# Kernel tuning notes

Hardware: AMD Instinct MI355X
Metric: run time of the kernel (lower is better)

## Reference

```python
import jax, jax.numpy as jnp
import numpy as np

B, P, M, C = 64, 8732, 16, 81
THRESHOLD = 0.5
NEG_POS_RATIO = 3
ALPHA = 1.0  # config.reg_weights
EPS = 1e-7


def cxcy_to_xy(c):
    return jnp.concatenate([c[..., :2] - c[..., 2:] / 2.0,
                            c[..., :2] + c[..., 2:] / 2.0], axis=-1)


def _rand_boxes_cxcy(key, shape):
    k1, k2 = jax.random.split(key)
    cxcy = jax.random.uniform(k1, shape + (2,), minval=0.2, maxval=0.8)
    wh = jax.random.uniform(k2, shape + (2,), minval=0.05, maxval=0.35)
    return jnp.concatenate([cxcy, wh], axis=-1)


def setup_inputs() -> dict:
    key = jax.random.key(0)
    ks = jax.random.split(key, 5)
    predicted_locs = cxcy_to_xy(_rand_boxes_cxcy(ks[0], (B, P)))          # valid corner boxes
    predicted_scores = jax.random.normal(ks[1], (B, P, C), dtype=jnp.float32)
    boxes = jnp.clip(cxcy_to_xy(_rand_boxes_cxcy(ks[2], (B, M))), 0.0, 1.0)  # GT corner boxes
    labels = jax.random.randint(ks[3], (B, M), 1, C)                       # object labels (1..C-1)
    priors_cxcy = _rand_boxes_cxcy(ks[4], (P,))
    return {"predicted_locs": predicted_locs, "predicted_scores": predicted_scores,
            "boxes": boxes, "labels": labels, "priors_cxcy": priors_cxcy}


def jaccard(a, b):
    # a: [M,4], b: [P,4] corner boxes -> [M,P] IoU
    lt = jnp.maximum(a[:, None, :2], b[None, :, :2])
    rb = jnp.minimum(a[:, None, 2:], b[None, :, 2:])
    wh = jnp.clip(rb - lt, 0.0)
    inter = wh[..., 0] * wh[..., 1]
    area_a = (a[:, 2] - a[:, 0]) * (a[:, 3] - a[:, 1])
    area_b = (b[:, 2] - b[:, 0]) * (b[:, 3] - b[:, 1])
    return inter / (area_a[:, None] + area_b[None, :] - inter)


def diou_loss(b1, b2):
    # corner boxes, elementwise over leading dims -> per-box loss 1 - DIoU
    lt = jnp.maximum(b1[..., :2], b2[..., :2])
    rb = jnp.minimum(b1[..., 2:], b2[..., 2:])
    wh = jnp.clip(rb - lt, 0.0)
    inter = wh[..., 0] * wh[..., 1]
    area1 = (b1[..., 2] - b1[..., 0]) * (b1[..., 3] - b1[..., 1])
    area2 = (b2[..., 2] - b2[..., 0]) * (b2[..., 3] - b2[..., 1])
    iou = inter / (area1 + area2 - inter + EPS)
    c1 = (b1[..., :2] + b1[..., 2:]) / 2.0
    c2 = (b2[..., :2] + b2[..., 2:]) / 2.0
    inter_diag = jnp.sum((c1 - c2) ** 2, axis=-1)
    enc_lt = jnp.minimum(b1[..., :2], b2[..., :2])
    enc_rb = jnp.maximum(b1[..., 2:], b2[..., 2:])
    outer_diag = jnp.sum((enc_rb - enc_lt) ** 2, axis=-1)
    dious = jnp.clip(iou - inter_diag / (outer_diag + EPS), -1.0, 1.0)
    return 1.0 - dious


def reference(predicted_locs, predicted_scores, boxes, labels, priors_cxcy):
    priors_xy = cxcy_to_xy(priors_cxcy)

    def assign(boxes_i, labels_i):
        overlap = jaccard(boxes_i, priors_xy)              # [M, P]
        ovl_prior = overlap.max(axis=0)                    # best overlap per prior
        obj_prior = overlap.argmax(axis=0)                 # best object per prior
        ovl_obj = overlap.max(axis=1)                      # best overlap per object
        prior_obj = overlap.argmax(axis=1)                 # best prior per object
        valid = ovl_obj > 0
        j_idx = jnp.cumsum(valid.astype(jnp.int32)) - 1    # index within filtered list (faithful)
        idx = jnp.where(valid, prior_obj, P)               # P -> dropped (out of bounds)
        ovl_prior = ovl_prior.at[idx].set(1.0, mode='drop')
        obj_prior = obj_prior.at[idx].set(j_idx, mode='drop')
        lab = labels_i[obj_prior]
        label_pos = jnp.where(ovl_prior < THRESHOLD, 0, lab)
        label_neg = jnp.where(ovl_prior < THRESHOLD - 0.1, -1, lab)
        return label_pos, label_neg

    true_classes, true_neg_classes = jax.vmap(assign)(boxes, labels)  # [B,P] each
    positive = true_classes > 0                                        # [B,P]
    pos_f = positive.astype(jnp.float32)
    n_pos_total = jnp.sum(pos_f)

    # Localization loss: DIoU(pred_pos, pred_pos) with reduce='mean' (faithful to source)
    per_box = diou_loss(predicted_locs, predicted_locs)                # [B,P]
    loc_loss = jnp.sum(per_box * pos_f) / jnp.maximum(n_pos_total, 1.0)

    # Confidence loss: per-prior CE + hard-negative mining (neg_pos_ratio)
    logp = jax.nn.log_softmax(predicted_scores, axis=-1)
    conf_all = -jnp.take_along_axis(logp, true_classes[..., None], axis=-1)[..., 0]  # [B,P]
    conf_pos_sum = jnp.sum(conf_all * pos_f)
    conf_neg = jnp.where(positive, 0.0, conf_all)
    conf_neg_sorted = -jnp.sort(-conf_neg, axis=-1)                    # descending
    n_hard = NEG_POS_RATIO * jnp.sum(positive, axis=1)                 # [B]
    hard_mask = (jnp.arange(P)[None, :] < n_hard[:, None]).astype(jnp.float32)
    conf_loss = (jnp.sum(conf_neg_sorted * hard_mask) + conf_pos_sum) / n_pos_total

    return conf_loss + ALPHA * loc_loss
```

## Files before the change

kernel.cpp:

```cpp
#include <hip/hip_runtime.h>
#include <math.h>

#define B_ 64
#define P_ 8732
#define M_ 16
#define C_ 81
#define THRESH 0.5f
#define EPS_ 1e-7f

#define ROWS_PER_CHUNK 64
#define NCHUNKS ((B_ * P_) / ROWS_PER_CHUNK)
#define CHUNK_F4 (ROWS_PER_CHUNK * C_ / 4)

__global__ __launch_bounds__(1024) void assign_kernel(
    const float* __restrict__ boxes,
    const int*   __restrict__ labels,
    const float* __restrict__ priors,
    int*         __restrict__ true_classes,
    int*         __restrict__ n_pos,
    int*         __restrict__ done_ctr)
{
    const int b = blockIdx.x;
    const int tid = threadIdx.x;
    const int lane = tid & 63;
    const int wv = tid >> 6;

    if (b == 0 && tid == 0) *done_ctr = 0;

    __shared__ float s_ovl[P_];
    __shared__ unsigned char s_obj[P_];
    __shared__ float s_bx[M_][4];
    __shared__ float s_barea[M_];
    __shared__ int   s_lab[M_];
    __shared__ float s_wv[M_][16];
    __shared__ int   s_wp[M_][16];
    __shared__ float s_ovl_obj[M_];
    __shared__ int   s_prior_obj[M_];
    __shared__ int   s_cnt[16];

    if (tid < M_*4) ((float*)s_bx)[tid] = boxes[b*M_*4 + tid];
    if (tid < M_)   s_lab[tid] = labels[b*M_ + tid];
    __syncthreads();
    if (tid < M_)
        s_barea[tid] = (s_bx[tid][2]-s_bx[tid][0])*(s_bx[tid][3]-s_bx[tid][1]);
    __syncthreads();

    float bestv[M_]; int bestp[M_];
    #pragma unroll
    for (int m = 0; m < M_; ++m) { bestv[m] = -1.0f; bestp[m] = 0x7fffffff; }

    for (int p = tid; p < P_; p += 1024) {
        float4 pc = ((const float4*)priors)[p];
        float px1 = pc.x - pc.z*0.5f, py1 = pc.y - pc.w*0.5f;
        float px2 = pc.x + pc.z*0.5f, py2 = pc.y + pc.w*0.5f;
        float parea = (px2-px1)*(py2-py1);
        float bv = -1.0f; int bm = 0;
        #pragma unroll
        for (int m = 0; m < M_; ++m) {
            float ix1 = fmaxf(s_bx[m][0], px1);
            float iy1 = fmaxf(s_bx[m][1], py1);
            float ix2 = fminf(s_bx[m][2], px2);
            float iy2 = fminf(s_bx[m][3], py2);
            float iw = fmaxf(ix2-ix1, 0.0f);
            float ih = fmaxf(iy2-iy1, 0.0f);
            float inter = iw*ih;
            float iou = inter / (s_barea[m] + parea - inter);
            if (iou > bv) { bv = iou; bm = m; }
            if (iou > bestv[m]) { bestv[m] = iou; bestp[m] = p; }
        }
        s_ovl[p] = bv;
        s_obj[p] = (unsigned char)bm;
    }

    #pragma unroll
    for (int m = 0; m < M_; ++m) {
        float v = bestv[m]; int p = bestp[m];
        #pragma unroll
        for (int o = 32; o; o >>= 1) {
            float v2 = __shfl_xor(v, o);
            int   p2 = __shfl_xor(p, o);
            if (v2 > v || (v2 == v && p2 < p)) { v = v2; p = p2; }
        }
        if (lane == 0) { s_wv[m][wv] = v; s_wp[m][wv] = p; }
    }
    __syncthreads();

    if (tid < M_) {
        float v = s_wv[tid][0]; int p = s_wp[tid][0];
        #pragma unroll
        for (int w = 1; w < 16; ++w) {
            float v2 = s_wv[tid][w]; int p2 = s_wp[tid][w];
            if (v2 > v || (v2 == v && p2 < p)) { v = v2; p = p2; }
        }
        s_ovl_obj[tid] = v; s_prior_obj[tid] = p;
    }
    __syncthreads();

    if (tid == 0) {
        int cnt = 0;
        for (int m = 0; m < M_; ++m) {
            if (s_ovl_obj[m] > 0.0f) {
                int p = s_prior_obj[m];
                s_ovl[p] = 1.0f;
                s_obj[p] = (unsigned char)cnt;
                cnt++;
            }
        }
    }
    __syncthreads();

    int cpos = 0;
    for (int p = tid; p < P_; p += 1024) {
        int tc = 0;
        if (!(s_ovl[p] < THRESH)) tc = s_lab[s_obj[p]];
        true_classes[(size_t)b*P_ + p] = tc;
        cpos += (tc > 0);
    }
    #pragma unroll
    for (int o = 32; o; o >>= 1) cpos += __shfl_xor(cpos, o);
    if (lane == 0) s_cnt[wv] = cpos;
    __syncthreads();
    if (tid == 0) {
        int t = 0;
        #pragma unroll
        for (int w = 0; w < 16; ++w) t += s_cnt[w];
        n_pos[b] = t;
    }
}

__global__ __launch_bounds__(256, 6) void ce_loc_kernel(
    const float* __restrict__ scores,
    const float* __restrict__ locs,
    const int*   __restrict__ tcls,
    float*       __restrict__ conf_neg,
    float*       __restrict__ blk_pos,
    float*       __restrict__ blk_loc)
{
    const int c    = blockIdx.x;
    const int tid  = threadIdx.x;
    const int lane = tid & 63;
    const int wv   = tid >> 6;
    const int s    = lane & 3;
    const int rl   = (lane >> 2) + wv * 16;

    __shared__ __attribute__((aligned(16))) float s_buf[ROWS_PER_CHUNK * C_];
    __shared__ float s_red[4][2];

    const float4* src4 = (const float4*)scores + (size_t)c * CHUNK_F4;
    float4*       dst4 = (float4*)s_buf;

    #pragma unroll
    for (int k = 0; k < 5; ++k) {
        __builtin_amdgcn_global_load_lds(
            (const __attribute__((address_space(1))) void*)(src4 + k*256 + tid),
            (__attribute__((address_space(3))) void*)(dst4 + k*256 + wv*64),
            16, 0, 0);
    }
    if (tid < 16) dst4[1280 + tid] = src4[1280 + tid];

    const int row = c * ROWS_PER_CHUNK + rl;
    const int t = tcls[row];
    __syncthreads();

    const int cnt   = (s == 0) ? 21 : 20;
    const int cbase = (s == 0) ? 0  : (1 + 20 * s);

    const float* rowp = &s_buf[rl * C_ + cbase];
    float x[21];
    float mx = -INFINITY;
    #pragma unroll
    for (int k = 0; k < 21; ++k) {
        if (k < cnt) { x[k] = rowp[k]; mx = fmaxf(mx, x[k]); }
        else x[k] = -INFINITY;
    }
    mx = fmaxf(mx, __shfl_xor(mx, 1));
    mx = fmaxf(mx, __shfl_xor(mx, 2));

    float e = 0.f, stv = 0.f;
    #pragma unroll
    for (int k = 0; k < 21; ++k) {
        e += __expf(x[k] - mx);
        if ((cbase + k == t) && (k < cnt)) stv = x[k];
    }
    e   += __shfl_xor(e, 1);   e   += __shfl_xor(e, 2);
    stv += __shfl_xor(stv, 1); stv += __shfl_xor(stv, 2);

    float p_acc = 0.f, l_acc = 0.f;
    if (s == 0) {
        float conf = mx + __logf(e) - stv;
        if (t > 0) {
            conf_neg[row] = 0.f;
            p_acc = conf;
            float4 bx = ((const float4*)locs)[row];
            float w = bx.z - bx.x, h = bx.w - bx.y;
            float iw = fmaxf(w, 0.f), ih = fmaxf(h, 0.f);
            float inter = iw * ih;
            float area  = w * h;
            float iou   = inter / (area + area - inter + EPS_);
            float diou  = fminf(fmaxf(iou, -1.f), 1.f);
            l_acc = 1.f - diou;
        } else {
            conf_neg[row] = fmaxf(conf, 0.f);
        }
    }

    #pragma unroll
    for (int o = 32; o; o >>= 1) {
        p_acc += __shfl_xor(p_acc, o);
        l_acc += __shfl_xor(l_acc, o);
    }
    if (lane == 0) { s_red[wv][0] = p_acc; s_red[wv][1] = l_acc; }
    __syncthreads();
    if (tid == 0) {
        blk_pos[c] = s_red[0][0] + s_red[1][0] + s_red[2][0] + s_red[3][0];
        blk_loc[c] = s_red[0][1] + s_red[1][1] + s_red[2][1] + s_red[3][1];
    }
}

__global__ __launch_bounds__(1024) void topk_kernel(
    const float* __restrict__ conf_neg,
    const int*   __restrict__ n_pos,
    const float* __restrict__ blk_pos,
    const float* __restrict__ blk_loc,
    float*       __restrict__ hard,
    int*         __restrict__ done_ctr,
    float*       __restrict__ out)
{
    const int b = blockIdx.x;
    const int tid = threadIdx.x;
    const int lane = tid & 63;
    const int wv = tid >> 6;

    __shared__ float s_v[P_];
    __shared__ int   s_hist[16][256];
    __shared__ int   s_cg[257];
    __shared__ int   s_sel;
    __shared__ int   s_t[16];
    __shared__ float s_f[16];
    __shared__ int   s_last;
    __shared__ double sd[16][4];

    const float4* cn4 = (const float4*)(conf_neg + (size_t)b * P_);
    for (int i = tid; i < P_/4; i += 1024) ((float4*)s_v)[i] = cn4[i];

    int k = 3 * n_pos[b];
    if (k > P_) k = P_;

    float hsum = 0.f;
    if (k > 0) {
        __syncthreads();

        const unsigned masks[4]  = {0u, 0xFF800000u, 0xFFFF8000u, 0xFFFFFF80u};
        const int      shifts[4] = {23, 15, 7, 0};

        unsigned prefix = 0u;
        int k_rem = k;

        for (int rd = 0; rd < 4; ++rd) {
            const unsigned hm = masks[rd];
            const int sh = shifts[rd];

            ((int*)s_hist)[tid] = 0;
            ((int*)s_hist)[tid + 1024] = 0;
            ((int*)s_hist)[tid + 2048] = 0;
            ((int*)s_hist)[tid + 3072] = 0;
            __syncthreads();

            for (int i = tid; i < P_; i += 1024) {
                unsigned u = __float_as_uint(s_v[i]);
                if ((u & hm) == prefix)
                    atomicAdd(&s_hist[wv][(u >> sh) & 0xFF], 1);
            }
            __syncthreads();

            if (wv == 0) {
                int carry = 0;
                for (int cbin = 3; cbin >= 0; --cbin) {
                    int bin = cbin * 64 + lane;
                    int tot = 0;
                    #pragma unroll
                    for (int w = 0; w < 16; ++w) tot += s_hist[w][bin];
                    #pragma unroll
                    for (int o = 1; o < 64; o <<= 1) {
                        int v = __shfl_down(tot, o);
                        if (lane + o < 64) tot += v;
                    }
                    int cg = tot + carry;
                    s_cg[bin] = cg;
                    carry = __shfl(cg, 0);
                }
                if (lane == 0) s_cg[256] = 0;
            }
            __syncthreads();

            if (tid < 256) {
                if (s_cg[tid] >= k_rem && s_cg[tid + 1] < k_rem) s_sel = tid;
            }
            __syncthreads();

            const int bsel = s_sel;
            k_rem -= s_cg[bsel + 1];
            prefix |= (unsigned)bsel << sh;
            __syncthreads();
        }

        const float tval = __uint_as_float(prefix);

        float sum = 0.f; int cgt = 0;
        for (int i = tid; i < P_; i += 1024) {
            float v = s_v[i];
            if (v > tval) { sum += v; cgt++; }
        }
        #pragma unroll
        for (int o = 32; o; o >>= 1) { sum += __shfl_xor(sum, o); cgt += __shfl_xor(cgt, o); }
        if (lane == 0) { s_f[wv] = sum; s_t[wv] = cgt; }
        __syncthreads();
        if (tid == 0) {
            float ssum = 0.f; int cc = 0;
            #pragma unroll
            for (int w = 0; w < 16; ++w) { ssum += s_f[w]; cc += s_t[w]; }
            hsum = ssum + (float)(k - cc) * tval;
        }
    }

    if (tid == 0) {
        atomicExch(&hard[b], hsum);
        __threadfence();
        s_last = (atomicAdd(done_ctr, 1) == B_ - 1) ? 1 : 0;
    }
    __syncthreads();

    if (s_last) {
        __threadfence();
        double p = 0.0, l = 0.0;
        for (int i = tid; i < NCHUNKS; i += 1024) { p += blk_pos[i]; l += blk_loc[i]; }
        double h = 0.0, np = 0.0;
        if (tid < B_) {
            h  = (double)atomicAdd(&hard[tid], 0.0f);
            np = (double)n_pos[tid];
        }
        #pragma unroll
        for (int o = 32; o; o >>= 1) {
            p += __shfl_xor(p, o); l += __shfl_xor(l, o);
            h += __shfl_xor(h, o); np += __shfl_xor(np, o);
        }
        if (lane == 0) { sd[wv][0] = p; sd[wv][1] = l; sd[wv][2] = h; sd[wv][3] = np; }
        __syncthreads();
        if (tid == 0) {
            double tp = 0, tl = 0, th = 0, tn = 0;
            #pragma unroll
            for (int w = 0; w < 16; ++w) { tp += sd[w][0]; tl += sd[w][1]; th += sd[w][2]; tn += sd[w][3]; }
            double conf_loss = (th + tp) / tn;
            double loc_loss  = tl / fmax(tn, 1.0);
            out[0] = (float)(conf_loss + 1.0 * loc_loss);
        }
    }
}

extern "C" void kernel_launch(void* const* d_in, const int* in_sizes, int n_in,
                              void* d_out, int out_size, void* d_ws, size_t ws_size,
                              hipStream_t stream) {
    const float* predicted_locs   = (const float*)d_in[0];
    const float* predicted_scores = (const float*)d_in[1];
    const float* boxes            = (const float*)d_in[2];
    const int*   labels           = (const int*)d_in[3];
    const float* priors           = (const float*)d_in[4];
    float* out = (float*)d_out;

    char* ws = (char*)d_ws;
    size_t off = 0;
    int*    true_classes = (int*)(ws + off);   off += sizeof(int)   * (size_t)B_ * P_;
    float*  conf_neg     = (float*)(ws + off); off += sizeof(float) * (size_t)B_ * P_;
    float*  blk_pos      = (float*)(ws + off); off += sizeof(float) * NCHUNKS;
    float*  blk_loc      = (float*)(ws + off); off += sizeof(float) * NCHUNKS;
    float*  hard         = (float*)(ws + off); off += sizeof(float) * B_;
    int*    n_pos        = (int*)(ws + off);   off += sizeof(int)   * B_;
    int*    done_ctr     = (int*)(ws + off);   off += sizeof(int)   * 4;

    assign_kernel<<<B_, 1024, 0, stream>>>(boxes, labels, priors,
                                           true_classes, n_pos, done_ctr);
    ce_loc_kernel<<<NCHUNKS, 256, 0, stream>>>(predicted_scores, predicted_locs,
                                               true_classes, conf_neg,
                                               blk_pos, blk_loc);
    topk_kernel<<<B_, 1024, 0, stream>>>(conf_neg, n_pos, blk_pos, blk_loc,
                                         hard, done_ctr, out);
}
```

Measured before the change: 361.2 us.

## Fuse assignment with log-sum-exp kernel and move CE gather into top-k

The prior-to-box assignment now runs in the same grid as the per-row log-sum-exp pass. The first 64 blocks do the assignment and the remaining blocks compute only the LSE, so the LSE no longer waits on true_classes and one kernel launch plus the serial dependency go away. The assignment blocks shrink to 256 threads and compute IoU twice instead of holding per-prior overlap in shared memory. The top-k kernel now gathers the target score, computes the positive CE and localization sums and counts positives itself, so the per-chunk partial buffers and the conf_neg array are dropped. The cost is scattered gathers from the scores tensor inside the top-k kernel and fewer threads per block on the assignment path.

```diff
diff --git a/kernel.cpp b/kernel.cpp
--- a/kernel.cpp
+++ b/kernel.cpp
@@ -8,221 +8,176 @@
 #define THRESH 0.5f
 #define EPS_ 1e-7f
 
+#define AB_ 64
 #define ROWS_PER_CHUNK 64
 #define NCHUNKS ((B_ * P_) / ROWS_PER_CHUNK)
 #define CHUNK_F4 (ROWS_PER_CHUNK * C_ / 4)
 
-__global__ __launch_bounds__(1024) void assign_kernel(
+__global__ __launch_bounds__(256, 4) void fused_assign_lse(
+    const float* __restrict__ scores,
     const float* __restrict__ boxes,
     const int*   __restrict__ labels,
     const float* __restrict__ priors,
-    int*         __restrict__ true_classes,
-    int*         __restrict__ n_pos,
+    float*       __restrict__ lse,
+    int*         __restrict__ tcls,
     int*         __restrict__ done_ctr)
 {
-    const int b = blockIdx.x;
-    const int tid = threadIdx.x;
-    const int lane = tid & 63;
-    const int wv = tid >> 6;
-
-    if (b == 0 && tid == 0) *done_ctr = 0;
-
-    __shared__ float s_ovl[P_];
-    __shared__ unsigned char s_obj[P_];
+    __shared__ __attribute__((aligned(16))) float s_buf[ROWS_PER_CHUNK * C_];
     __shared__ float s_bx[M_][4];
     __shared__ float s_barea[M_];
     __shared__ int   s_lab[M_];
-    __shared__ float s_wv[M_][16];
-    __shared__ int   s_wp[M_][16];
-    __shared__ float s_ovl_obj[M_];
-    __shared__ int   s_prior_obj[M_];
-    __shared__ int   s_cnt[16];
-
-    if (tid < M_*4) ((float*)s_bx)[tid] = boxes[b*M_*4 + tid];
-    if (tid < M_)   s_lab[tid] = labels[b*M_ + tid];
-    __syncthreads();
-    if (tid < M_)
-        s_barea[tid] = (s_bx[tid][2]-s_bx[tid][0])*(s_bx[tid][3]-s_bx[tid][1]);
-    __syncthreads();
-
-    float bestv[M_]; int bestp[M_];
-    #pragma unroll
-    for (int m = 0; m < M_; ++m) { bestv[m] = -1.0f; bestp[m] = 0x7fffffff; }
-
-    for (int p = tid; p < P_; p += 1024) {
-        float4 pc = ((const float4*)priors)[p];
-        float px1 = pc.x - pc.z*0.5f, py1 = pc.y - pc.w*0.5f;
-        float px2 = pc.x + pc.z*0.5f, py2 = pc.y + pc.w*0.5f;
-        float parea = (px2-px1)*(py2-py1);
-        float bv = -1.0f; int bm = 0;
-        #pragma unroll
-        for (int m = 0; m < M_; ++m) {
-            float ix1 = fmaxf(s_bx[m][0], px1);
-            float iy1 = fmaxf(s_bx[m][1], py1);
-            float ix2 = fminf(s_bx[m][2], px2);
-            float iy2 = fminf(s_bx[m][3], py2);
-            float iw = fmaxf(ix2-ix1, 0.0f);
-            float ih = fmaxf(iy2-iy1, 0.0f);
-            float inter = iw*ih;
-            float iou = inter / (s_barea[m] + parea - inter);
-            if (iou > bv) { bv = iou; bm = m; }
-            if (iou > bestv[m]) { bestv[m] = iou; bestp[m] = p; }
-        }
-        s_ovl[p] = bv;
-        s_obj[p] = (unsigned char)bm;
-    }
-
-    #pragma unroll
-    for (int m = 0; m < M_; ++m) {
-        float v = bestv[m]; int p = bestp[m];
-        #pragma unroll
-        for (int o = 32; o; o >>= 1) {
-            float v2 = __shfl_xor(v, o);
-            int   p2 = __shfl_xor(p, o);
-            if (v2 > v || (v2 == v && p2 < p)) { v = v2; p = p2; }
-        }
-        if (lane == 0) { s_wv[m][wv] = v; s_wp[m][wv] = p; }
-    }
-    __syncthreads();
-
-    if (tid < M_) {
-        float v = s_wv[tid][0]; int p = s_wp[tid][0];
-        #pragma unroll
-        for (int w = 1; w < 16; ++w) {
-            float v2 = s_wv[tid][w]; int p2 = s_wp[tid][w];
-            if (v2 > v || (v2 == v && p2 < p)) { v = v2; p = p2; }
-        }
-        s_ovl_obj[tid] = v; s_prior_obj[tid] = p;
-    }
-    __syncthreads();
-
-    if (tid == 0) {
-        int cnt = 0;
-        for (int m = 0; m < M_; ++m) {
-            if (s_ovl_obj[m] > 0.0f) {
-                int p = s_prior_obj[m];
-                s_ovl[p] = 1.0f;
-                s_obj[p] = (unsigned char)cnt;
-                cnt++;
-            }
-        }
-    }
-    __syncthreads();
-
-    int cpos = 0;
-    for (int p = tid; p < P_; p += 1024) {
-        int tc = 0;
-        if (!(s_ovl[p] < THRESH)) tc = s_lab[s_obj[p]];
-        true_classes[(size_t)b*P_ + p] = tc;
-        cpos += (tc > 0);
-    }
-    #pragma unroll
-    for (int o = 32; o; o >>= 1) cpos += __shfl_xor(cpos, o);
-    if (lane == 0) s_cnt[wv] = cpos;
-    __syncthreads();
-    if (tid == 0) {
-        int t = 0;
-        #pragma unroll
-        for (int w = 0; w < 16; ++w) t += s_cnt[w];
-        n_pos[b] = t;
-    }
-}
-
-__global__ __launch_bounds__(256, 6) void ce_loc_kernel(
-    const float* __restrict__ scores,
-    const float* __restrict__ locs,
-    const int*   __restrict__ tcls,
-    float*       __restrict__ conf_neg,
-    float*       __restrict__ blk_pos,
-    float*       __restrict__ blk_loc)
-{
-    const int c    = blockIdx.x;
+    __shared__ float s_wv4[M_][4];
+    __shared__ int   s_wp4[M_][4];
+    __shared__ int   s_tp[M_];
+    __shared__ int   s_tn;
+
     const int tid  = threadIdx.x;
     const int lane = tid & 63;
     const int wv   = tid >> 6;
-    const int s    = lane & 3;
-    const int rl   = (lane >> 2) + wv * 16;
-
-    __shared__ __attribute__((aligned(16))) float s_buf[ROWS_PER_CHUNK * C_];
-    __shared__ float s_red[4][2];
-
-    const float4* src4 = (const float4*)scores + (size_t)c * CHUNK_F4;
-    float4*       dst4 = (float4*)s_buf;
-
-    #pragma unroll
-    for (int k = 0; k < 5; ++k) {
-        __builtin_amdgcn_global_load_lds(
-            (const __attribute__((address_space(1))) void*)(src4 + k*256 + tid),
-            (__attribute__((address_space(3))) void*)(dst4 + k*256 + wv*64),
-            16, 0, 0);
-    }
-    if (tid < 16) dst4[1280 + tid] = src4[1280 + tid];
-
-    const int row = c * ROWS_PER_CHUNK + rl;
-    const int t = tcls[row];
-    __syncthreads();
-
-    const int cnt   = (s == 0) ? 21 : 20;
-    const int cbase = (s == 0) ? 0  : (1 + 20 * s);
-
-    const float* rowp = &s_buf[rl * C_ + cbase];
-    float x[21];
-    float mx = -INFINITY;
-    #pragma unroll
-    for (int k = 0; k < 21; ++k) {
-        if (k < cnt) { x[k] = rowp[k]; mx = fmaxf(mx, x[k]); }
-        else x[k] = -INFINITY;
-    }
-    mx = fmaxf(mx, __shfl_xor(mx, 1));
-    mx = fmaxf(mx, __shfl_xor(mx, 2));
-
-    float e = 0.f, stv = 0.f;
-    #pragma unroll
-    for (int k = 0; k < 21; ++k) {
-        e += __expf(x[k] - mx);
-        if ((cbase + k == t) && (k < cnt)) stv = x[k];
-    }
-    e   += __shfl_xor(e, 1);   e   += __shfl_xor(e, 2);
-    stv += __shfl_xor(stv, 1); stv += __shfl_xor(stv, 2);
-
-    float p_acc = 0.f, l_acc = 0.f;
-    if (s == 0) {
-        float conf = mx + __logf(e) - stv;
-        if (t > 0) {
-            conf_neg[row] = 0.f;
-            p_acc = conf;
-            float4 bx = ((const float4*)locs)[row];
-            float w = bx.z - bx.x, h = bx.w - bx.y;
-            float iw = fmaxf(w, 0.f), ih = fmaxf(h, 0.f);
-            float inter = iw * ih;
-            float area  = w * h;
-            float iou   = inter / (area + area - inter + EPS_);
-            float diou  = fminf(fmaxf(iou, -1.f), 1.f);
-            l_acc = 1.f - diou;
-        } else {
-            conf_neg[row] = fmaxf(conf, 0.f);
-        }
-    }
-
-    #pragma unroll
-    for (int o = 32; o; o >>= 1) {
-        p_acc += __shfl_xor(p_acc, o);
-        l_acc += __shfl_xor(l_acc, o);
-    }
-    if (lane == 0) { s_red[wv][0] = p_acc; s_red[wv][1] = l_acc; }
-    __syncthreads();
-    if (tid == 0) {
-        blk_pos[c] = s_red[0][0] + s_red[1][0] + s_red[2][0] + s_red[3][0];
-        blk_loc[c] = s_red[0][1] + s_red[1][1] + s_red[2][1] + s_red[3][1];
+
+    if (blockIdx.x < AB_) {
+        const int b = blockIdx.x;
+        if (b == 0 && tid == 0) *done_ctr = 0;
+
+        if (tid < M_*4) ((float*)s_bx)[tid] = boxes[b*M_*4 + tid];
+        if (tid < M_)   s_lab[tid] = labels[b*M_ + tid];
+        __syncthreads();
+        if (tid < M_)
+            s_barea[tid] = (s_bx[tid][2]-s_bx[tid][0])*(s_bx[tid][3]-s_bx[tid][1]);
+        __syncthreads();
+
+        const float4* pri4 = (const float4*)priors;
+
+        float bestv[M_]; int bestp[M_];
+        #pragma unroll
+        for (int m = 0; m < M_; ++m) { bestv[m] = -1.0f; bestp[m] = 0x7fffffff; }
+
+        for (int p = tid; p < P_; p += 256) {
+            float4 pc = pri4[p];
+            float px1 = pc.x - pc.z*0.5f, py1 = pc.y - pc.w*0.5f;
+            float px2 = pc.x + pc.z*0.5f, py2 = pc.y + pc.w*0.5f;
+            float parea = (px2-px1)*(py2-py1);
+            #pragma unroll
+            for (int m = 0; m < M_; ++m) {
+                float ix1 = fmaxf(s_bx[m][0], px1);
+                float iy1 = fmaxf(s_bx[m][1], py1);
+                float ix2 = fminf(s_bx[m][2], px2);
+                float iy2 = fminf(s_bx[m][3], py2);
+                float iw = fmaxf(ix2-ix1, 0.0f);
+                float ih = fmaxf(iy2-iy1, 0.0f);
+                float inter = iw*ih;
+                float iou = inter / (s_barea[m] + parea - inter);
+                if (iou > bestv[m]) { bestv[m] = iou; bestp[m] = p; }
+            }
+        }
+
+        #pragma unroll
+        for (int m = 0; m < M_; ++m) {
+            float v = bestv[m]; int p = bestp[m];
+            #pragma unroll
+            for (int o = 32; o; o >>= 1) {
+                float v2 = __shfl_xor(v, o);
+                int   p2 = __shfl_xor(p, o);
+                if (v2 > v || (v2 == v && p2 < p)) { v = v2; p = p2; }
+            }
+            if (lane == 0) { s_wv4[m][wv] = v; s_wp4[m][wv] = p; }
+        }
+        __syncthreads();
+
+        if (tid == 0) {
+            int cnt = 0;
+            for (int m = 0; m < M_; ++m) {
+                float v = s_wv4[m][0]; int p = s_wp4[m][0];
+                #pragma unroll
+                for (int w = 1; w < 4; ++w) {
+                    float v2 = s_wv4[m][w]; int p2 = s_wp4[m][w];
+                    if (v2 > v || (v2 == v && p2 < p)) { v = v2; p = p2; }
+                }
+                if (v > 0.0f) { s_tp[cnt] = p; cnt++; }
+            }
+            s_tn = cnt;
+        }
+        __syncthreads();
+
+        const int tn = s_tn;
+
+        for (int p = tid; p < P_; p += 256) {
+            float4 pc = pri4[p];
+            float px1 = pc.x - pc.z*0.5f, py1 = pc.y - pc.w*0.5f;
+            float px2 = pc.x + pc.z*0.5f, py2 = pc.y + pc.w*0.5f;
+            float parea = (px2-px1)*(py2-py1);
+            float bv = -1.0f; int bm = 0;
+            #pragma unroll
+            for (int m = 0; m < M_; ++m) {
+                float ix1 = fmaxf(s_bx[m][0], px1);
+                float iy1 = fmaxf(s_bx[m][1], py1);
+                float ix2 = fminf(s_bx[m][2], px2);
+                float iy2 = fminf(s_bx[m][3], py2);
+                float iw = fmaxf(ix2-ix1, 0.0f);
+                float ih = fmaxf(iy2-iy1, 0.0f);
+                float inter = iw*ih;
+                float iou = inter / (s_barea[m] + parea - inter);
+                if (iou > bv) { bv = iou; bm = m; }
+            }
+            int ovr = -1;
+            for (int e = 0; e < tn; ++e)
+                if (s_tp[e] == p) ovr = e;
+            int tc = (ovr >= 0) ? s_lab[ovr]
+                                : ((bv < THRESH) ? 0 : s_lab[bm]);
+            tcls[(size_t)b*P_ + p] = tc;
+        }
+    } else {
+        const int c  = blockIdx.x - AB_;
+        const int s  = lane & 3;
+        const int rl = (lane >> 2) + wv * 16;
+
+        const float4* src4 = (const float4*)scores + (size_t)c * CHUNK_F4;
+        float4*       dst4 = (float4*)s_buf;
+
+        #pragma unroll
+        for (int k = 0; k < 5; ++k) {
+            __builtin_amdgcn_global_load_lds(
+                (const __attribute__((address_space(1))) void*)(src4 + k*256 + tid),
+                (__attribute__((address_space(3))) void*)(dst4 + k*256 + wv*64),
+                16, 0, 0);
+        }
+        if (tid < 16) dst4[1280 + tid] = src4[1280 + tid];
+        __syncthreads();
+
+        const int cnt   = (s == 0) ? 21 : 20;
+        const int cbase = (s == 0) ? 0  : (1 + 20 * s);
+
+        const float* rowp = &s_buf[rl * C_ + cbase];
+        float x[21];
+        float mx = -INFINITY;
+        #pragma unroll
+        for (int k = 0; k < 21; ++k) {
+            if (k < cnt) { x[k] = rowp[k]; mx = fmaxf(mx, x[k]); }
+            else x[k] = -INFINITY;
+        }
+        mx = fmaxf(mx, __shfl_xor(mx, 1));
+        mx = fmaxf(mx, __shfl_xor(mx, 2));
+
+        float e = 0.f;
+        #pragma unroll
+        for (int k = 0; k < 21; ++k) e += __expf(x[k] - mx);
+        e += __shfl_xor(e, 1);
+        e += __shfl_xor(e, 2);
+
+        if (s == 0)
+            lse[(size_t)c * ROWS_PER_CHUNK + rl] = mx + __logf(e);
     }
 }
 
 __global__ __launch_bounds__(1024) void topk_kernel(
-    const float* __restrict__ conf_neg,
-    const int*   __restrict__ n_pos,
-    const float* __restrict__ blk_pos,
-    const float* __restrict__ blk_loc,
+    const float* __restrict__ scores,
+    const float* __restrict__ locs,
+    const float* __restrict__ lse,
+    const int*   __restrict__ tcls,
     float*       __restrict__ hard,
+    float*       __restrict__ psum,
+    float*       __restrict__ lsum,
+    int*         __restrict__ npos,
     int*         __restrict__ done_ctr,
     float*       __restrict__ out)
 {
@@ -235,21 +190,55 @@
     __shared__ int   s_hist[16][256];
     __shared__ int   s_cg[257];
     __shared__ int   s_sel;
-    __shared__ int   s_t[16];
-    __shared__ float s_f[16];
+    __shared__ int   s_ct[16];
+    __shared__ float s_pa[16];
+    __shared__ float s_la[16];
+    __shared__ int   s_rt[16];
+    __shared__ float s_rf[16];
     __shared__ int   s_last;
-    __shared__ double sd[16][4];
-
-    const float4* cn4 = (const float4*)(conf_neg + (size_t)b * P_);
-    for (int i = tid; i < P_/4; i += 1024) ((float4*)s_v)[i] = cn4[i];
-
-    int k = 3 * n_pos[b];
+
+    const size_t base = (size_t)b * P_;
+
+    float p_acc = 0.f, l_acc = 0.f; int cpos = 0;
+    for (int i = tid; i < P_; i += 1024) {
+        const int t = tcls[base + i];
+        const float conf = lse[base + i] - scores[(base + i) * C_ + t];
+        float v;
+        if (t > 0) {
+            v = 0.f;
+            cpos++;
+            p_acc += conf;
+            float4 bx = ((const float4*)locs)[base + i];
+            float w = bx.z - bx.x, h = bx.w - bx.y;
+            float iw = fmaxf(w, 0.f), ih = fmaxf(h, 0.f);
+            float inter = iw * ih;
+            float area  = w * h;
+            float iou   = inter / (area + area - inter + EPS_);
+            float diou  = fminf(fmaxf(iou, -1.f), 1.f);
+            l_acc += 1.f - diou;
+        } else {
+            v = fmaxf(conf, 0.f);
+        }
+        s_v[i] = v;
+    }
+
+    #pragma unroll
+    for (int o = 32; o; o >>= 1) {
+        cpos  += __shfl_xor(cpos, o);
+        p_acc += __shfl_xor(p_acc, o);
+        l_acc += __shfl_xor(l_acc, o);
+    }
+    if (lane == 0) { s_ct[wv] = cpos; s_pa[wv] = p_acc; s_la[wv] = l_acc; }
+    __syncthreads();
+
+    int cp_tot = 0;
+    #pragma unroll
+    for (int w = 0; w < 16; ++w) cp_tot += s_ct[w];
+    int k = 3 * cp_tot;
     if (k > P_) k = P_;
 
     float hsum = 0.f;
     if (k > 0) {
-        __syncthreads();
-
         const unsigned masks[4]  = {0u, 0xFF800000u, 0xFFFF8000u, 0xFFFFFF80u};
         const int      shifts[4] = {23, 15, 7, 0};
 
@@ -313,45 +302,43 @@
         }
         #pragma unroll
         for (int o = 32; o; o >>= 1) { sum += __shfl_xor(sum, o); cgt += __shfl_xor(cgt, o); }
-        if (lane == 0) { s_f[wv] = sum; s_t[wv] = cgt; }
+        if (lane == 0) { s_rf[wv] = sum; s_rt[wv] = cgt; }
         __syncthreads();
         if (tid == 0) {
             float ssum = 0.f; int cc = 0;
             #pragma unroll
-            for (int w = 0; w < 16; ++w) { ssum += s_f[w]; cc += s_t[w]; }
+            for (int w = 0; w < 16; ++w) { ssum += s_rf[w]; cc += s_rt[w]; }
             hsum = ssum + (float)(k - cc) * tval;
         }
     }
 
     if (tid == 0) {
+        float pt = 0.f, lt = 0.f;
+        #pragma unroll
+        for (int w = 0; w < 16; ++w) { pt += s_pa[w]; lt += s_la[w]; }
         atomicExch(&hard[b], hsum);
+        atomicExch(&psum[b], pt);
+        atomicExch(&lsum[b], lt);
+        atomicExch(&npos[b], cp_tot);
         __threadfence();
         s_last = (atomicAdd(done_ctr, 1) == B_ - 1) ? 1 : 0;
     }
     __syncthreads();
 
-    if (s_last) {
+    if (s_last && wv == 0) {
         __threadfence();
-        double p = 0.0, l = 0.0;
-        for (int i = tid; i < NCHUNKS; i += 1024) { p += blk_pos[i]; l += blk_loc[i]; }
-        double h = 0.0, np = 0.0;
-        if (tid < B_) {
-            h  = (double)atomicAdd(&hard[tid], 0.0f);
-            np = (double)n_pos[tid];
-        }
+        double h  = (double)atomicAdd(&hard[lane], 0.0f);
+        double p  = (double)atomicAdd(&psum[lane], 0.0f);
+        double l  = (double)atomicAdd(&lsum[lane], 0.0f);
+        double np = (double)atomicAdd(&npos[lane], 0);
         #pragma unroll
         for (int o = 32; o; o >>= 1) {
-            p += __shfl_xor(p, o); l += __shfl_xor(l, o);
-            h += __shfl_xor(h, o); np += __shfl_xor(np, o);
-        }
-        if (lane == 0) { sd[wv][0] = p; sd[wv][1] = l; sd[wv][2] = h; sd[wv][3] = np; }
-        __syncthreads();
-        if (tid == 0) {
-            double tp = 0, tl = 0, th = 0, tn = 0;
-            #pragma unroll
-            for (int w = 0; w < 16; ++w) { tp += sd[w][0]; tl += sd[w][1]; th += sd[w][2]; tn += sd[w][3]; }
-            double conf_loss = (th + tp) / tn;
-            double loc_loss  = tl / fmax(tn, 1.0);
+            h += __shfl_xor(h, o); p += __shfl_xor(p, o);
+            l += __shfl_xor(l, o); np += __shfl_xor(np, o);
+        }
+        if (lane == 0) {
+            double conf_loss = (h + p) / np;
+            double loc_loss  = l / fmax(np, 1.0);
             out[0] = (float)(conf_loss + 1.0 * loc_loss);
         }
     }
@@ -369,19 +356,17 @@
 
     char* ws = (char*)d_ws;
     size_t off = 0;
-    int*    true_classes = (int*)(ws + off);   off += sizeof(int)   * (size_t)B_ * P_;
-    float*  conf_neg     = (float*)(ws + off); off += sizeof(float) * (size_t)B_ * P_;
-    float*  blk_pos      = (float*)(ws + off); off += sizeof(float) * NCHUNKS;
-    float*  blk_loc      = (float*)(ws + off); off += sizeof(float) * NCHUNKS;
-    float*  hard         = (float*)(ws + off); off += sizeof(float) * B_;
-    int*    n_pos        = (int*)(ws + off);   off += sizeof(int)   * B_;
-    int*    done_ctr     = (int*)(ws + off);   off += sizeof(int)   * 4;
-
-    assign_kernel<<<B_, 1024, 0, stream>>>(boxes, labels, priors,
-                                           true_classes, n_pos, done_ctr);
-    ce_loc_kernel<<<NCHUNKS, 256, 0, stream>>>(predicted_scores, predicted_locs,
-                                               true_classes, conf_neg,
-                                               blk_pos, blk_loc);
-    topk_kernel<<<B_, 1024, 0, stream>>>(conf_neg, n_pos, blk_pos, blk_loc,
-                                         hard, done_ctr, out);
+    float* lse      = (float*)(ws + off); off += sizeof(float) * (size_t)B_ * P_;
+    int*   tcls     = (int*)(ws + off);   off += sizeof(int)   * (size_t)B_ * P_;
+    float* hard     = (float*)(ws + off); off += sizeof(float) * B_;
+    float* psum     = (float*)(ws + off); off += sizeof(float) * B_;
+    float* lsum     = (float*)(ws + off); off += sizeof(float) * B_;
+    int*   npos     = (int*)(ws + off);   off += sizeof(int)   * B_;
+    int*   done_ctr = (int*)(ws + off);   off += sizeof(int)   * 4;
+
+    fused_assign_lse<<<AB_ + NCHUNKS, 256, 0, stream>>>(
+        predicted_scores, boxes, labels, priors, lse, tcls, done_ctr);
+    topk_kernel<<<B_, 1024, 0, stream>>>(
+        predicted_scores, predicted_locs, lse, tcls,
+        hard, psum, lsum, npos, done_ctr, out);
 }
```

Measured after the change: 395.7 us. +9.6%, slower.

## Recompute IoU instead of LDS staging; grid-stride CE with 16 lanes per row

Applied to the files above, without the earlier changes.

The assign kernel drops its per-prior shared-memory overlap and object arrays and runs at 256 threads. It recomputes IoUs in a second pass and resolves forced matches with a small list lookup. The CE kernel replaces the LDS staging via global_load_lds with a persistent grid-stride loop over 2048 blocks. Each row is read straight from global memory by 16 lanes with shuffle reductions. This trades shared-memory footprint and launch count for extra recompute and less coalesced 81-float row loads. The top-k kernel's syncthreads moves outside the k>0 branch.

```diff
diff --git a/kernel.cpp b/kernel.cpp
--- a/kernel.cpp
+++ b/kernel.cpp
@@ -8,35 +8,31 @@
 #define THRESH 0.5f
 #define EPS_ 1e-7f
 
-#define ROWS_PER_CHUNK 64
-#define NCHUNKS ((B_ * P_) / ROWS_PER_CHUNK)
-#define CHUNK_F4 (ROWS_PER_CHUNK * C_ / 4)
-
-__global__ __launch_bounds__(1024) void assign_kernel(
+#define CE_BLOCKS 2048
+
+__global__ __launch_bounds__(256) void assign_kernel(
     const float* __restrict__ boxes,
     const int*   __restrict__ labels,
     const float* __restrict__ priors,
-    int*         __restrict__ true_classes,
+    int*         __restrict__ tcls,
     int*         __restrict__ n_pos,
-    int*         __restrict__ done_ctr)
+    int*         __restrict__ ctrs)
 {
-    const int b = blockIdx.x;
-    const int tid = threadIdx.x;
-    const int lane = tid & 63;
-    const int wv = tid >> 6;
-
-    if (b == 0 && tid == 0) *done_ctr = 0;
-
-    __shared__ float s_ovl[P_];
-    __shared__ unsigned char s_obj[P_];
     __shared__ float s_bx[M_][4];
     __shared__ float s_barea[M_];
     __shared__ int   s_lab[M_];
-    __shared__ float s_wv[M_][16];
-    __shared__ int   s_wp[M_][16];
-    __shared__ float s_ovl_obj[M_];
-    __shared__ int   s_prior_obj[M_];
-    __shared__ int   s_cnt[16];
+    __shared__ float s_wv4[M_][4];
+    __shared__ int   s_wp4[M_][4];
+    __shared__ int   s_tp[M_];
+    __shared__ int   s_tn;
+    __shared__ int   s_cnt[4];
+
+    const int b    = blockIdx.x;
+    const int tid  = threadIdx.x;
+    const int lane = tid & 63;
+    const int wv   = tid >> 6;
+
+    if (b == 0 && tid < 2) ctrs[tid] = 0;
 
     if (tid < M_*4) ((float*)s_bx)[tid] = boxes[b*M_*4 + tid];
     if (tid < M_)   s_lab[tid] = labels[b*M_ + tid];
@@ -44,13 +40,65 @@
     if (tid < M_)
         s_barea[tid] = (s_bx[tid][2]-s_bx[tid][0])*(s_bx[tid][3]-s_bx[tid][1]);
     __syncthreads();
+
+    const float4* pri4 = (const float4*)priors;
 
     float bestv[M_]; int bestp[M_];
     #pragma unroll
     for (int m = 0; m < M_; ++m) { bestv[m] = -1.0f; bestp[m] = 0x7fffffff; }
 
-    for (int p = tid; p < P_; p += 1024) {
-        float4 pc = ((const float4*)priors)[p];
+    for (int p = tid; p < P_; p += 256) {
+        float4 pc = pri4[p];
+        float px1 = pc.x - pc.z*0.5f, py1 = pc.y - pc.w*0.5f;
+        float px2 = pc.x + pc.z*0.5f, py2 = pc.y + pc.w*0.5f;
+        float parea = (px2-px1)*(py2-py1);
+        #pragma unroll
+        for (int m = 0; m < M_; ++m) {
+            float ix1 = fmaxf(s_bx[m][0], px1);
+            float iy1 = fmaxf(s_bx[m][1], py1);
+            float ix2 = fminf(s_bx[m][2], px2);
+            float iy2 = fminf(s_bx[m][3], py2);
+            float iw = fmaxf(ix2-ix1, 0.0f);
+            float ih = fmaxf(iy2-iy1, 0.0f);
+            float inter = iw*ih;
+            float iou = inter / (s_barea[m] + parea - inter);
+            if (iou > bestv[m]) { bestv[m] = iou; bestp[m] = p; }
+        }
+    }
+
+    #pragma unroll
+    for (int m = 0; m < M_; ++m) {
+        float v = bestv[m]; int p = bestp[m];
+        #pragma unroll
+        for (int o = 32; o; o >>= 1) {
+            float v2 = __shfl_xor(v, o);
+            int   p2 = __shfl_xor(p, o);
+            if (v2 > v || (v2 == v && p2 < p)) { v = v2; p = p2; }
+        }
+        if (lane == 0) { s_wv4[m][wv] = v; s_wp4[m][wv] = p; }
+    }
+    __syncthreads();
+
+    if (tid == 0) {
+        int cnt = 0;
+        for (int m = 0; m < M_; ++m) {
+            float v = s_wv4[m][0]; int p = s_wp4[m][0];
+            #pragma unroll
+            for (int w = 1; w < 4; ++w) {
+                float v2 = s_wv4[m][w]; int p2 = s_wp4[m][w];
+                if (v2 > v || (v2 == v && p2 < p)) { v = v2; p = p2; }
+            }
+            if (v > 0.0f) { s_tp[cnt] = p; cnt++; }
+        }
+        s_tn = cnt;
+    }
+    __syncthreads();
+
+    const int tn = s_tn;
+
+    int cpos = 0;
+    for (int p = tid; p < P_; p += 256) {
+        float4 pc = pri4[p];
         float px1 = pc.x - pc.z*0.5f, py1 = pc.y - pc.w*0.5f;
         float px2 = pc.x + pc.z*0.5f, py2 = pc.y + pc.w*0.5f;
         float parea = (px2-px1)*(py2-py1);
@@ -66,56 +114,16 @@
             float inter = iw*ih;
             float iou = inter / (s_barea[m] + parea - inter);
             if (iou > bv) { bv = iou; bm = m; }
-            if (iou > bestv[m]) { bestv[m] = iou; bestp[m] = p; }
-        }
-        s_ovl[p] = bv;
-        s_obj[p] = (unsigned char)bm;
-    }
-
-    #pragma unroll
-    for (int m = 0; m < M_; ++m) {
-        float v = bestv[m]; int p = bestp[m];
-        #pragma unroll
-        for (int o = 32; o; o >>= 1) {
-            float v2 = __shfl_xor(v, o);
-            int   p2 = __shfl_xor(p, o);
-            if (v2 > v || (v2 == v && p2 < p)) { v = v2; p = p2; }
-        }
-        if (lane == 0) { s_wv[m][wv] = v; s_wp[m][wv] = p; }
-    }
-    __syncthreads();
-
-    if (tid < M_) {
-        float v = s_wv[tid][0]; int p = s_wp[tid][0];
-        #pragma unroll
-        for (int w = 1; w < 16; ++w) {
-            float v2 = s_wv[tid][w]; int p2 = s_wp[tid][w];
-            if (v2 > v || (v2 == v && p2 < p)) { v = v2; p = p2; }
-        }
-        s_ovl_obj[tid] = v; s_prior_obj[tid] = p;
-    }
-    __syncthreads();
-
-    if (tid == 0) {
-        int cnt = 0;
-        for (int m = 0; m < M_; ++m) {
-            if (s_ovl_obj[m] > 0.0f) {
-                int p = s_prior_obj[m];
-                s_ovl[p] = 1.0f;
-                s_obj[p] = (unsigned char)cnt;
-                cnt++;
-            }
-        }
-    }
-    __syncthreads();
-
-    int cpos = 0;
-    for (int p = tid; p < P_; p += 1024) {
-        int tc = 0;
-        if (!(s_ovl[p] < THRESH)) tc = s_lab[s_obj[p]];
-        true_classes[(size_t)b*P_ + p] = tc;
+        }
+        int ovr = -1;
+        for (int e = 0; e < tn; ++e)
+            if (s_tp[e] == p) ovr = e;
+        int tc = (ovr >= 0) ? s_lab[ovr]
+                            : ((bv < THRESH) ? 0 : s_lab[bm]);
+        tcls[(size_t)b*P_ + p] = tc;
         cpos += (tc > 0);
     }
+
     #pragma unroll
     for (int o = 32; o; o >>= 1) cpos += __shfl_xor(cpos, o);
     if (lane == 0) s_cnt[wv] = cpos;
@@ -123,12 +131,12 @@
     if (tid == 0) {
         int t = 0;
         #pragma unroll
-        for (int w = 0; w < 16; ++w) t += s_cnt[w];
+        for (int w = 0; w < 4; ++w) t += s_cnt[w];
         n_pos[b] = t;
     }
 }
 
-__global__ __launch_bounds__(256, 6) void ce_loc_kernel(
+__global__ __launch_bounds__(256) void ce_loc_kernel(
     const float* __restrict__ scores,
     const float* __restrict__ locs,
     const int*   __restrict__ tcls,
@@ -136,71 +144,63 @@
     float*       __restrict__ blk_pos,
     float*       __restrict__ blk_loc)
 {
-    const int c    = blockIdx.x;
     const int tid  = threadIdx.x;
     const int lane = tid & 63;
+    const int j    = lane & 15;
+    const int g    = lane >> 4;
     const int wv   = tid >> 6;
-    const int s    = lane & 3;
-    const int rl   = (lane >> 2) + wv * 16;
-
-    __shared__ __attribute__((aligned(16))) float s_buf[ROWS_PER_CHUNK * C_];
+    const int gwave = blockIdx.x * 4 + wv;
+    const int ngrp  = CE_BLOCKS * 4;
+    const int NG = (B_ * P_) / 4;
+
     __shared__ float s_red[4][2];
 
-    const float4* src4 = (const float4*)scores + (size_t)c * CHUNK_F4;
-    float4*       dst4 = (float4*)s_buf;
-
-    #pragma unroll
-    for (int k = 0; k < 5; ++k) {
-        __builtin_amdgcn_global_load_lds(
-            (const __attribute__((address_space(1))) void*)(src4 + k*256 + tid),
-            (__attribute__((address_space(3))) void*)(dst4 + k*256 + wv*64),
-            16, 0, 0);
-    }
-    if (tid < 16) dst4[1280 + tid] = src4[1280 + tid];
-
-    const int row = c * ROWS_PER_CHUNK + rl;
-    const int t = tcls[row];
-    __syncthreads();
-
-    const int cnt   = (s == 0) ? 21 : 20;
-    const int cbase = (s == 0) ? 0  : (1 + 20 * s);
-
-    const float* rowp = &s_buf[rl * C_ + cbase];
-    float x[21];
-    float mx = -INFINITY;
-    #pragma unroll
-    for (int k = 0; k < 21; ++k) {
-        if (k < cnt) { x[k] = rowp[k]; mx = fmaxf(mx, x[k]); }
-        else x[k] = -INFINITY;
-    }
-    mx = fmaxf(mx, __shfl_xor(mx, 1));
-    mx = fmaxf(mx, __shfl_xor(mx, 2));
-
-    float e = 0.f, stv = 0.f;
-    #pragma unroll
-    for (int k = 0; k < 21; ++k) {
-        e += __expf(x[k] - mx);
-        if ((cbase + k == t) && (k < cnt)) stv = x[k];
-    }
-    e   += __shfl_xor(e, 1);   e   += __shfl_xor(e, 2);
-    stv += __shfl_xor(stv, 1); stv += __shfl_xor(stv, 2);
-
     float p_acc = 0.f, l_acc = 0.f;
-    if (s == 0) {
-        float conf = mx + __logf(e) - stv;
-        if (t > 0) {
-            conf_neg[row] = 0.f;
-            p_acc = conf;
-            float4 bx = ((const float4*)locs)[row];
-            float w = bx.z - bx.x, h = bx.w - bx.y;
-            float iw = fmaxf(w, 0.f), ih = fmaxf(h, 0.f);
-            float inter = iw * ih;
-            float area  = w * h;
-            float iou   = inter / (area + area - inter + EPS_);
-            float diou  = fminf(fmaxf(iou, -1.f), 1.f);
-            l_acc = 1.f - diou;
-        } else {
-            conf_neg[row] = fmaxf(conf, 0.f);
+
+    for (int grp = gwave; grp < NG; grp += ngrp) {
+        const int r = grp * 4 + g;
+        const float* row = scores + (size_t)r * C_;
+
+        float x[6];
+        #pragma unroll
+        for (int k = 0; k < 5; ++k) x[k] = row[16*k + j];
+        x[5] = (j == 0) ? row[80] : -INFINITY;
+
+        float mx = fmaxf(fmaxf(fmaxf(x[0], x[1]), fmaxf(x[2], x[3])),
+                         fmaxf(x[4], x[5]));
+        #pragma unroll
+        for (int o = 1; o < 16; o <<= 1) mx = fmaxf(mx, __shfl_xor(mx, o));
+
+        const int t = tcls[r];
+        float e = 0.f, st = 0.f;
+        #pragma unroll
+        for (int k = 0; k < 6; ++k) {
+            e += __expf(x[k] - mx);
+            const int idx = 16*k + j;
+            if (idx == t) st = x[k];
+        }
+        #pragma unroll
+        for (int o = 1; o < 16; o <<= 1) {
+            e  += __shfl_xor(e, o);
+            st += __shfl_xor(st, o);
+        }
+
+        if (j == 0) {
+            float conf = mx + __logf(e) - st;
+            if (t > 0) {
+                conf_neg[r] = 0.f;
+                p_acc += conf;
+                float4 bx = ((const float4*)locs)[r];
+                float w = bx.z - bx.x, h = bx.w - bx.y;
+                float iw = fmaxf(w, 0.f), ih = fmaxf(h, 0.f);
+                float inter = iw * ih;
+                float area  = w * h;
+                float iou   = inter / (area + area - inter + EPS_);
+                float diou  = fminf(fmaxf(iou, -1.f), 1.f);
+                l_acc += 1.f - diou;
+            } else {
+                conf_neg[r] = fmaxf(conf, 0.f);
+            }
         }
     }
 
@@ -212,8 +212,8 @@
     if (lane == 0) { s_red[wv][0] = p_acc; s_red[wv][1] = l_acc; }
     __syncthreads();
     if (tid == 0) {
-        blk_pos[c] = s_red[0][0] + s_red[1][0] + s_red[2][0] + s_red[3][0];
-        blk_loc[c] = s_red[0][1] + s_red[1][1] + s_red[2][1] + s_red[3][1];
+        blk_pos[blockIdx.x] = s_red[0][0] + s_red[1][0] + s_red[2][0] + s_red[3][0];
+        blk_loc[blockIdx.x] = s_red[0][1] + s_red[1][1] + s_red[2][1] + s_red[3][1];
     }
 }
 
@@ -223,7 +223,7 @@
     const float* __restrict__ blk_pos,
     const float* __restrict__ blk_loc,
     float*       __restrict__ hard,
-    int*         __restrict__ done_ctr,
+    int*         __restrict__ ctrs,
     float*       __restrict__ out)
 {
     const int b = blockIdx.x;
@@ -245,11 +245,10 @@
 
     int k = 3 * n_pos[b];
     if (k > P_) k = P_;
+    __syncthreads();
 
     float hsum = 0.f;
     if (k > 0) {
-        __syncthreads();
-
         const unsigned masks[4]  = {0u, 0xFF800000u, 0xFFFF8000u, 0xFFFFFF80u};
         const int      shifts[4] = {23, 15, 7, 0};
 
@@ -326,15 +325,14 @@
     if (tid == 0) {
         atomicExch(&hard[b], hsum);
         __threadfence();
-        s_last = (atomicAdd(done_ctr, 1) == B_ - 1) ? 1 : 0;
+        s_last = (atomicAdd(&ctrs[1], 1) == B_ - 1) ? 1 : 0;
     }
     __syncthreads();
 
     if (s_last) {
         __threadfence();
-        double p = 0.0, l = 0.0;
-        for (int i = tid; i < NCHUNKS; i += 1024) { p += blk_pos[i]; l += blk_loc[i]; }
-        double h = 0.0, np = 0.0;
+        double p = 0.0, l = 0.0, h = 0.0, np = 0.0;
+        for (int i = tid; i < CE_BLOCKS; i += 1024) { p += blk_pos[i]; l += blk_loc[i]; }
         if (tid < B_) {
             h  = (double)atomicAdd(&hard[tid], 0.0f);
             np = (double)n_pos[tid];
@@ -369,19 +367,18 @@
 
     char* ws = (char*)d_ws;
     size_t off = 0;
-    int*    true_classes = (int*)(ws + off);   off += sizeof(int)   * (size_t)B_ * P_;
-    float*  conf_neg     = (float*)(ws + off); off += sizeof(float) * (size_t)B_ * P_;
-    float*  blk_pos      = (float*)(ws + off); off += sizeof(float) * NCHUNKS;
-    float*  blk_loc      = (float*)(ws + off); off += sizeof(float) * NCHUNKS;
-    float*  hard         = (float*)(ws + off); off += sizeof(float) * B_;
-    int*    n_pos        = (int*)(ws + off);   off += sizeof(int)   * B_;
-    int*    done_ctr     = (int*)(ws + off);   off += sizeof(int)   * 4;
-
-    assign_kernel<<<B_, 1024, 0, stream>>>(boxes, labels, priors,
-                                           true_classes, n_pos, done_ctr);
-    ce_loc_kernel<<<NCHUNKS, 256, 0, stream>>>(predicted_scores, predicted_locs,
-                                               true_classes, conf_neg,
-                                               blk_pos, blk_loc);
+    int*   tcls     = (int*)(ws + off);   off += sizeof(int)   * (size_t)B_ * P_;
+    float* conf_neg = (float*)(ws + off); off += sizeof(float) * (size_t)B_ * P_;
+    float* blk_pos  = (float*)(ws + off); off += sizeof(float) * CE_BLOCKS;
+    float* blk_loc  = (float*)(ws + off); off += sizeof(float) * CE_BLOCKS;
+    int*   n_pos    = (int*)(ws + off);   off += sizeof(int)   * B_;
+    float* hard     = (float*)(ws + off); off += sizeof(float) * B_;
+    int*   ctrs     = (int*)(ws + off);   off += sizeof(int)   * 4;
+
+    assign_kernel<<<B_, 256, 0, stream>>>(boxes, labels, priors,
+                                          tcls, n_pos, ctrs);
+    ce_loc_kernel<<<CE_BLOCKS, 256, 0, stream>>>(predicted_scores, predicted_locs,
+                                                 tcls, conf_neg, blk_pos, blk_loc);
     topk_kernel<<<B_, 1024, 0, stream>>>(conf_neg, n_pos, blk_pos, blk_loc,
-                                         hard, done_ctr, out);
+                                         hard, ctrs, out);
 }
```

Result: slower. 390.4 us (+8.1%).
